# Kernel optimization log

Hardware: AMD Instinct MI355X
Metric: run time of the kernel (lower is better)

Reference implementation:

```python
import jax, jax.numpy as jnp
import numpy as np

N, D = 4096, 2048

def setup_inputs() -> dict:
    key = jax.random.key(0)
    k1, k2 = jax.random.split(key)
    Ws = jax.random.normal(k1, (N, D), dtype=jnp.float32)
    # nn.Bilinear(D, D, 1): weight [1, D, D], bias [1]
    W = jax.random.normal(k2, (1, D, D), dtype=jnp.float32) * (1.0 / np.sqrt(D))
    b = jnp.zeros((1,), dtype=jnp.float32)
    return {"Ws": Ws, "W": W, "b": b}

def reference(Ws, W, b):
    # A[i, j] = Ws[i] @ W[0] @ Ws[j] + b[0]  (bilinear score for every pair)
    t = Ws @ W[0]                 # [N, D]
    A = t @ Ws.T + b[0]           # [N, N]
    return jax.nn.softmax(A, axis=1)
```

## Files before the change

### kernel.cpp

```cpp
#include <hip/hip_runtime.h>

typedef __bf16 bf16x8 __attribute__((ext_vector_type(8)));
typedef float f32x4 __attribute__((ext_vector_type(4)));
typedef unsigned short u16;
typedef u16 u16x8 __attribute__((ext_vector_type(8)));

#define AS1 __attribute__((address_space(1)))
#define AS3 __attribute__((address_space(3)))
#define MF(d, a, b) d = __builtin_amdgcn_mfma_f32_16x16x32_bf16(a, b, d, 0, 0, 0)

__device__ __forceinline__ void split2(float x, u16& h, u16& l) {
  __bf16 hb = (__bf16)x;
  float hf = (float)hb;
  __bf16 lb = (__bf16)(x - hf);
  h = __builtin_bit_cast(u16, hb);
  l = __builtin_bit_cast(u16, lb);
}

__global__ __launch_bounds__(256) void k_pack_ws(const float* __restrict__ X,
                                                 u16* __restrict__ P) {
  const int total8 = (4096 * 2048) / 8;
  for (int idx = blockIdx.x * 256 + threadIdx.x; idx < total8; idx += gridDim.x * 256) {
    int row = idx >> 8;
    int k8  = idx & 255;
    const float* src = X + ((size_t)row << 11) + (k8 << 3);
    const float4 v0 = *(const float4*)src;
    const float4 v1 = *(const float4*)(src + 4);
    float xv[8] = {v0.x, v0.y, v0.z, v0.w, v1.x, v1.y, v1.z, v1.w};
    u16x8 hv, lv;
#pragma unroll
    for (int j = 0; j < 8; ++j) { u16 h, l; split2(xv[j], h, l); hv[j] = h; lv[j] = l; }
    size_t base = ((size_t)row << 12) + (size_t)((k8 >> 2) << 6) + ((k8 & 3) << 3);
    *(u16x8*)(P + base) = hv;
    *(u16x8*)(P + base + 32) = lv;
  }
}

__global__ __launch_bounds__(256) void k_transpose_pack_w(const float* __restrict__ W,
                                                          u16* __restrict__ P) {
  __shared__ float tile[32][33];
  const int tx = threadIdx.x, ty = threadIdx.y;
  const int kbase = blockIdx.y << 5, cbase = blockIdx.x << 5;
#pragma unroll
  for (int i = 0; i < 4; ++i)
    tile[ty * 4 + i][tx] = W[((size_t)(kbase + ty * 4 + i) << 11) + cbase + tx];
  __syncthreads();
#pragma unroll
  for (int i = 0; i < 4; ++i) {
    int c = cbase + ty * 4 + i;
    float v = tile[tx][ty * 4 + i];
    u16 h, l; split2(v, h, l);
    size_t base = ((size_t)c << 12) + (size_t)(kbase << 1) + tx;
    P[base] = h;
    P[base + 32] = l;
  }
}

__global__ __launch_bounds__(256, 2) void k_gemm_nt(const u16* __restrict__ Ap,
                                                    const u16* __restrict__ Bp,
                                                    u16* __restrict__ Cpack) {
  __shared__ __align__(16) u16 lds_a[128 * 64];
  __shared__ __align__(16) u16 lds_b[128 * 64];
  const int bid = blockIdx.x;
  const int swzb = (bid & 7) * 64 + (bid >> 3);
  const int bx = swzb & 15, by = swzb >> 4;
  const int tid = threadIdx.x;
  const int lane = tid & 63, w = tid >> 6;
  const int wr = w >> 1, wc = w & 1;
  const int row0 = by << 7, col0 = bx << 7;
  const int lrow = lane & 15, kg = lane >> 4;

  f32x4 acc[4][4] = {};

  const u16* abase = Ap + ((size_t)row0 << 12);
  const u16* bbase = Bp + ((size_t)col0 << 12);

  int offAh[4], offAl[4], offBh[4], offBl[4];
#pragma unroll
  for (int m = 0; m < 4; ++m) {
    int r = wr * 64 + m * 16 + lrow;
    int sw = r & 7;
    offAh[m] = r * 64 + ((kg ^ sw) << 3);
    offAl[m] = r * 64 + (((4 + kg) ^ sw) << 3);
    int rb = wc * 64 + m * 16 + lrow;
    int swb = rb & 7;
    offBh[m] = rb * 64 + ((kg ^ swb) << 3);
    offBl[m] = rb * 64 + (((4 + kg) ^ swb) << 3);
  }

  for (int kb = 0; kb < 64; ++kb) {
    const int kofs = kb << 6;
#pragma unroll
    for (int i = 0; i < 4; ++i) {
      int s = i * 256 + tid;
      int r = s >> 3, c = s & 7;
      int cs = c ^ (r & 7);
      __builtin_amdgcn_global_load_lds(
          (const AS1 unsigned int*)(abase + ((size_t)r << 12) + kofs + (cs << 3)),
          (AS3 unsigned int*)(lds_a + ((i * 256 + w * 64) << 3)), 16, 0, 0);
    }
#pragma unroll
    for (int i = 0; i < 4; ++i) {
      int s = i * 256 + tid;
      int r = s >> 3, c = s & 7;
      int cs = c ^ (r & 7);
      __builtin_amdgcn_global_load_lds(
          (const AS1 unsigned int*)(bbase + ((size_t)r << 12) + kofs + (cs << 3)),
          (AS3 unsigned int*)(lds_b + ((i * 256 + w * 64) << 3)), 16, 0, 0);
    }
    __syncthreads();

    bf16x8 ah[4], al[4];
#pragma unroll
    for (int m = 0; m < 4; ++m) {
      ah[m] = *(const bf16x8*)&lds_a[offAh[m]];
      al[m] = *(const bf16x8*)&lds_a[offAl[m]];
    }
#pragma unroll
    for (int n = 0; n < 4; ++n) {
      bf16x8 bh = *(const bf16x8*)&lds_b[offBh[n]];
      bf16x8 bl = *(const bf16x8*)&lds_b[offBl[n]];
#pragma unroll
      for (int m = 0; m < 4; ++m) {
        MF(acc[m][n], ah[m], bh);
        MF(acc[m][n], ah[m], bl);
        MF(acc[m][n], al[m], bh);
      }
    }
    __syncthreads();
  }

#pragma unroll
  for (int m = 0; m < 4; ++m) {
#pragma unroll
    for (int n = 0; n < 4; ++n) {
#pragma unroll
      for (int j = 0; j < 4; ++j) {
        int gr = row0 + wr * 64 + m * 16 + kg * 4 + j;
        int gc = col0 + wc * 64 + n * 16 + lrow;
        u16 h, l; split2(acc[m][n][j], h, l);
        size_t base = ((size_t)gr << 12) + (size_t)((gc >> 5) << 6) + (gc & 31);
        Cpack[base] = h;
        Cpack[base + 32] = l;
      }
    }
  }
}

__global__ __launch_bounds__(512, 2) void k_gemm256(const u16* __restrict__ Ap,
                                                    const u16* __restrict__ Bp,
                                                    float* __restrict__ Cout) {
  __shared__ __align__(16) u16 smA[32768];
  const int bid = blockIdx.x;
  const int swzb = (bid & 7) * 32 + (bid >> 3);
  const int bx = swzb & 15, by = swzb >> 4;
  const int tid = threadIdx.x;
  const int lane = tid & 63, w = tid >> 6;
  const int wr = w >> 2, wc = w & 3;
  const int row0 = by << 8, col0 = bx << 8;
  const int lrow = lane & 15, kg = lane >> 4;
  const int sw = lrow & 7;

  const u16* Abase = Ap + ((size_t)row0 << 12);
  const u16* Bbase = Bp + ((size_t)col0 << 12);

  const size_t gsrc0 = ((size_t)(tid >> 3) << 12) + ((size_t)((tid & 7) ^ ((tid >> 3) & 7)) << 3);
  const int dst0 = (w * 64) << 3;

  auto stA = [&](int T, int j) {
    __builtin_amdgcn_global_load_lds(
        (const AS1 unsigned int*)(Abase + gsrc0 + ((size_t)(j * 64) << 12) + ((T & 63) << 6)),
        (AS3 unsigned int*)(smA + ((T & 1) << 14) + j * 4096 + dst0), 16, 0, 0);
  };
  auto ldB = [&](int T, bf16x8* BH, bf16x8* BL) {
    const u16* src = Bbase + ((T & 63) << 6) + (kg << 3);
#pragma unroll
    for (int n = 0; n < 4; ++n) {
      size_t c = (size_t)(wc * 64 + n * 16 + lrow) << 12;
      BH[n] = *(const bf16x8*)(src + c);
      BL[n] = *(const bf16x8*)(src + c + 32);
    }
  };

  const int baseAh = (wr * 128 + lrow) * 64 + ((kg ^ sw) << 3);
  const int baseAl = (wr * 128 + lrow) * 64 + (((4 | kg) ^ sw) << 3);

  f32x4 acc[8][4] = {};
  bf16x8 bhE[4], blE[4], bhO[4], blO[4];

  stA(0, 0); stA(0, 1); stA(0, 2); stA(0, 3);
  ldB(0, bhE, blE);
  ldB(1, bhO, blO);
  __builtin_amdgcn_sched_barrier(0);
  asm volatile("s_waitcnt vmcnt(8)" ::: "memory");
  __builtin_amdgcn_sched_barrier(0);
  __builtin_amdgcn_s_barrier();

  for (int i = 0; i < 32; ++i) {
    const int t0 = 2 * i;
    const u16* laE = smA;
    const u16* laO = smA + 16384;
#pragma unroll
    for (int q = 0; q < 4; ++q) {
      bf16x8 a0h = *(const bf16x8*)&laE[baseAh + (2 * q) * 1024];
      bf16x8 a0l = *(const bf16x8*)&laE[baseAl + (2 * q) * 1024];
      bf16x8 a1h = *(const bf16x8*)&laE[baseAh + (2 * q + 1) * 1024];
      bf16x8 a1l = *(const bf16x8*)&laE[baseAl + (2 * q + 1) * 1024];
      if (q == 0) { stA(t0 + 1, 0); stA(t0 + 1, 1); }
      if (q == 1) { stA(t0 + 1, 2); stA(t0 + 1, 3); }
      __builtin_amdgcn_s_barrier();
      __builtin_amdgcn_s_setprio(1);
      const int m0 = 2 * q, m1 = 2 * q + 1;
#pragma unroll
      for (int n = 0; n < 4; ++n) { MF(acc[m0][n], a0h, bhE[n]); MF(acc[m1][n], a1h, bhE[n]); }
#pragma unroll
      for (int n = 0; n < 4; ++n) { MF(acc[m0][n], a0h, blE[n]); MF(acc[m1][n], a1h, blE[n]); }
#pragma unroll
      for (int n = 0; n < 4; ++n) { MF(acc[m0][n], a0l, bhE[n]); MF(acc[m1][n], a1l, bhE[n]); }
      __builtin_amdgcn_s_setprio(0);
      if (q == 3) {
        ldB(t0 + 2, bhE, blE);
        __builtin_amdgcn_sched_barrier(0);
        asm volatile("s_waitcnt vmcnt(8)" ::: "memory");
        __builtin_amdgcn_sched_barrier(0);
      }
      __builtin_amdgcn_s_barrier();
    }
#pragma unroll
    for (int q = 0; q < 4; ++q) {
      bf16x8 a0h = *(const bf16x8*)&laO[baseAh + (2 * q) * 1024];
      bf16x8 a0l = *(const bf16x8*)&laO[baseAl + (2 * q) * 1024];
      bf16x8 a1h = *(const bf16x8*)&laO[baseAh + (2 * q + 1) * 1024];
      bf16x8 a1l = *(const bf16x8*)&laO[baseAl + (2 * q + 1) * 1024];
      if (q == 0) { stA(t0 + 2, 0); stA(t0 + 2, 1); }
      if (q == 1) { stA(t0 + 2, 2); stA(t0 + 2, 3); }
      __builtin_amdgcn_s_barrier();
      __builtin_amdgcn_s_setprio(1);
      const int m0 = 2 * q, m1 = 2 * q + 1;
#pragma unroll
      for (int n = 0; n < 4; ++n) { MF(acc[m0][n], a0h, bhO[n]); MF(acc[m1][n], a1h, bhO[n]); }
#pragma unroll
      for (int n = 0; n < 4; ++n) { MF(acc[m0][n], a0h, blO[n]); MF(acc[m1][n], a1h, blO[n]); }
#pragma unroll
      for (int n = 0; n < 4; ++n) { MF(acc[m0][n], a0l, bhO[n]); MF(acc[m1][n], a1l, bhO[n]); }
      __builtin_amdgcn_s_setprio(0);
      if (q == 3) {
        ldB(t0 + 3, bhO, blO);
        __builtin_amdgcn_sched_barrier(0);
        asm volatile("s_waitcnt vmcnt(8)" ::: "memory");
        __builtin_amdgcn_sched_barrier(0);
      }
      __builtin_amdgcn_s_barrier();
    }
  }
  asm volatile("s_waitcnt vmcnt(0)" ::: "memory");

#pragma unroll
  for (int m = 0; m < 8; ++m) {
#pragma unroll
    for (int n = 0; n < 4; ++n) {
#pragma unroll
      for (int j = 0; j < 4; ++j) {
        int gr = row0 + wr * 128 + m * 16 + kg * 4 + j;
        int gc = col0 + wc * 64 + n * 16 + lrow;
        Cout[((size_t)gr << 12) + gc] = acc[m][n][j];
      }
    }
  }
}

__global__ __launch_bounds__(256) void k_softmax_rows(float* __restrict__ A) {
  const int row = blockIdx.x;
  float* p = A + ((size_t)row << 12);
  const int tid = threadIdx.x;
  const int lane = tid & 63, w = tid >> 6;
  float4 v[4];
  float mx = -3.0e38f;
#pragma unroll
  for (int i = 0; i < 4; ++i) {
    v[i] = ((const float4*)p)[tid + (i << 8)];
    mx = fmaxf(mx, fmaxf(fmaxf(v[i].x, v[i].y), fmaxf(v[i].z, v[i].w)));
  }
#pragma unroll
  for (int off = 32; off; off >>= 1) mx = fmaxf(mx, __shfl_xor(mx, off, 64));
  __shared__ float redm[4], reds[4];
  if (lane == 0) redm[w] = mx;
  __syncthreads();
  mx = fmaxf(fmaxf(redm[0], redm[1]), fmaxf(redm[2], redm[3]));
  float s = 0.f;
#pragma unroll
  for (int i = 0; i < 4; ++i) {
    v[i].x = __expf(v[i].x - mx);
    v[i].y = __expf(v[i].y - mx);
    v[i].z = __expf(v[i].z - mx);
    v[i].w = __expf(v[i].w - mx);
    s += (v[i].x + v[i].y) + (v[i].z + v[i].w);
  }
#pragma unroll
  for (int off = 32; off; off >>= 1) s += __shfl_xor(s, off, 64);
  if (lane == 0) reds[w] = s;
  __syncthreads();
  s = (reds[0] + reds[1]) + (reds[2] + reds[3]);
  const float inv = 1.0f / s;
#pragma unroll
  for (int i = 0; i < 4; ++i) {
    v[i].x *= inv; v[i].y *= inv; v[i].z *= inv; v[i].w *= inv;
    ((float4*)p)[tid + (i << 8)] = v[i];
  }
}

extern "C" void kernel_launch(void* const* d_in, const int* in_sizes, int n_in,
                              void* d_out, int out_size, void* d_ws, size_t ws_size,
                              hipStream_t stream) {
  (void)in_sizes; (void)n_in; (void)out_size; (void)ws_size;
  const float* Ws = (const float*)d_in[0];
  const float* W  = (const float*)d_in[1];
  float* out = (float*)d_out;

  u16* ws_pack = (u16*)d_ws;
  u16* wt_pack = ws_pack + (size_t)4096 * 4096;
  u16* t_pack  = wt_pack + (size_t)2048 * 4096;

  k_pack_ws<<<4096, 256, 0, stream>>>(Ws, ws_pack);
  k_transpose_pack_w<<<dim3(64, 64), dim3(32, 8), 0, stream>>>(W, wt_pack);
  k_gemm_nt<<<512, 256, 0, stream>>>(ws_pack, wt_pack, t_pack);
  k_gemm256<<<256, 512, 0, stream>>>(t_pack, ws_pack, out);
  k_softmax_rows<<<4096, 256, 0, stream>>>(out);
}
```

Measured before the change: 322.5 us.

## Replace 256x256 gemm with 128x256 tile staging both operands through LDS

```diff
diff --git a/kernel.cpp b/kernel.cpp
--- a/kernel.cpp
+++ b/kernel.cpp
@@ -147,17 +147,18 @@
   }
 }
 
-__global__ __launch_bounds__(512, 2) void k_gemm256(const u16* __restrict__ Ap,
-                                                    const u16* __restrict__ Bp,
-                                                    float* __restrict__ Cout) {
-  __shared__ __align__(16) u16 smA[32768];
+__global__ __launch_bounds__(512, 4) void k_gemm2(const u16* __restrict__ Ap,
+                                                  const u16* __restrict__ Bp,
+                                                  float* __restrict__ Cout) {
+  __shared__ __align__(16) u16 smA[16384];
+  __shared__ __align__(16) u16 smB[16384];
   const int bid = blockIdx.x;
-  const int swzb = (bid & 7) * 32 + (bid >> 3);
+  const int swzb = (bid & 7) * 64 + (bid >> 3);
   const int bx = swzb & 15, by = swzb >> 4;
   const int tid = threadIdx.x;
   const int lane = tid & 63, w = tid >> 6;
   const int wr = w >> 2, wc = w & 3;
-  const int row0 = by << 8, col0 = bx << 8;
+  const int row0 = by << 7, col0 = bx << 8;
   const int lrow = lane & 15, kg = lane >> 4;
   const int sw = lrow & 7;
 
@@ -165,103 +166,79 @@
   const u16* Bbase = Bp + ((size_t)col0 << 12);
 
   const size_t gsrc0 = ((size_t)(tid >> 3) << 12) + ((size_t)((tid & 7) ^ ((tid >> 3) & 7)) << 3);
-  const int dst0 = (w * 64) << 3;
+  const int dst0 = w * 512;
 
   auto stA = [&](int T, int j) {
     __builtin_amdgcn_global_load_lds(
         (const AS1 unsigned int*)(Abase + gsrc0 + ((size_t)(j * 64) << 12) + ((T & 63) << 6)),
-        (AS3 unsigned int*)(smA + ((T & 1) << 14) + j * 4096 + dst0), 16, 0, 0);
+        (AS3 unsigned int*)(smA + ((T & 1) << 13) + j * 4096 + dst0), 16, 0, 0);
   };
-  auto ldB = [&](int T, bf16x8* BH, bf16x8* BL) {
-    const u16* src = Bbase + ((T & 63) << 6) + (kg << 3);
-#pragma unroll
-    for (int n = 0; n < 4; ++n) {
-      size_t c = (size_t)(wc * 64 + n * 16 + lrow) << 12;
-      BH[n] = *(const bf16x8*)(src + c);
-      BL[n] = *(const bf16x8*)(src + c + 32);
-    }
+  auto stB = [&](int T, int u) {
+    __builtin_amdgcn_global_load_lds(
+        (const AS1 unsigned int*)(Bbase + gsrc0 + ((size_t)(u * 64) << 12) + ((T & 63) << 6)),
+        (AS3 unsigned int*)(smB + u * 4096 + dst0), 16, 0, 0);
   };
 
-  const int baseAh = (wr * 128 + lrow) * 64 + ((kg ^ sw) << 3);
-  const int baseAl = (wr * 128 + lrow) * 64 + (((4 | kg) ^ sw) << 3);
-
-  f32x4 acc[8][4] = {};
-  bf16x8 bhE[4], blE[4], bhO[4], blO[4];
-
-  stA(0, 0); stA(0, 1); stA(0, 2); stA(0, 3);
-  ldB(0, bhE, blE);
-  ldB(1, bhO, blO);
-  __builtin_amdgcn_sched_barrier(0);
-  asm volatile("s_waitcnt vmcnt(8)" ::: "memory");
+  const int baseAh = (wr * 64 + lrow) * 64 + ((kg ^ sw) << 3);
+  const int baseAl = (wr * 64 + lrow) * 64 + (((4 | kg) ^ sw) << 3);
+  int offBh[4], offBl[4];
+#pragma unroll
+  for (int n = 0; n < 4; ++n) {
+    offBh[n] = (wc * 64 + n * 16 + lrow) * 64 + ((kg ^ sw) << 3);
+    offBl[n] = (wc * 64 + n * 16 + lrow) * 64 + (((4 | kg) ^ sw) << 3);
+  }
+
+  f32x4 acc[4][4] = {};
+  bf16x8 bh[4], bl[4];
+
+  stA(0, 0); stA(0, 1);
+  stB(0, 0); stB(0, 1); stB(0, 2); stB(0, 3);
+  asm volatile("s_waitcnt vmcnt(0)" ::: "memory");
   __builtin_amdgcn_sched_barrier(0);
   __builtin_amdgcn_s_barrier();
 
-  for (int i = 0; i < 32; ++i) {
-    const int t0 = 2 * i;
-    const u16* laE = smA;
-    const u16* laO = smA + 16384;
+  for (int t = 0; t < 64; ++t) {
+    const u16* abuf = smA + ((t & 1) << 13);
 #pragma unroll
     for (int q = 0; q < 4; ++q) {
-      bf16x8 a0h = *(const bf16x8*)&laE[baseAh + (2 * q) * 1024];
-      bf16x8 a0l = *(const bf16x8*)&laE[baseAl + (2 * q) * 1024];
-      bf16x8 a1h = *(const bf16x8*)&laE[baseAh + (2 * q + 1) * 1024];
-      bf16x8 a1l = *(const bf16x8*)&laE[baseAl + (2 * q + 1) * 1024];
-      if (q == 0) { stA(t0 + 1, 0); stA(t0 + 1, 1); }
-      if (q == 1) { stA(t0 + 1, 2); stA(t0 + 1, 3); }
+      if (q == 0) {
+#pragma unroll
+        for (int n = 0; n < 4; ++n) {
+          bh[n] = *(const bf16x8*)&smB[offBh[n]];
+          bl[n] = *(const bf16x8*)&smB[offBl[n]];
+        }
+      }
+      bf16x8 ah = *(const bf16x8*)&abuf[baseAh + q * 1024];
+      bf16x8 al = *(const bf16x8*)&abuf[baseAl + q * 1024];
+      if (q == 0) { stA(t + 1, 0); stA(t + 1, 1); }
+      if (q == 1) { stB(t + 1, 0); stB(t + 1, 1); }
+      if (q == 2) { stB(t + 1, 2); stB(t + 1, 3); }
       __builtin_amdgcn_s_barrier();
       __builtin_amdgcn_s_setprio(1);
-      const int m0 = 2 * q, m1 = 2 * q + 1;
-#pragma unroll
-      for (int n = 0; n < 4; ++n) { MF(acc[m0][n], a0h, bhE[n]); MF(acc[m1][n], a1h, bhE[n]); }
-#pragma unroll
-      for (int n = 0; n < 4; ++n) { MF(acc[m0][n], a0h, blE[n]); MF(acc[m1][n], a1h, blE[n]); }
-#pragma unroll
-      for (int n = 0; n < 4; ++n) { MF(acc[m0][n], a0l, bhE[n]); MF(acc[m1][n], a1l, bhE[n]); }
+#pragma unroll
+      for (int n = 0; n < 4; ++n) MF(acc[q][n], ah, bh[n]);
+#pragma unroll
+      for (int n = 0; n < 4; ++n) MF(acc[q][n], ah, bl[n]);
+#pragma unroll
+      for (int n = 0; n < 4; ++n) MF(acc[q][n], al, bh[n]);
       __builtin_amdgcn_s_setprio(0);
+      asm volatile("s_waitcnt lgkmcnt(0)" ::: "memory");
+      __builtin_amdgcn_sched_barrier(0);
       if (q == 3) {
-        ldB(t0 + 2, bhE, blE);
+        asm volatile("s_waitcnt vmcnt(0)" ::: "memory");
         __builtin_amdgcn_sched_barrier(0);
-        asm volatile("s_waitcnt vmcnt(8)" ::: "memory");
-        __builtin_amdgcn_sched_barrier(0);
       }
       __builtin_amdgcn_s_barrier();
     }
-#pragma unroll
-    for (int q = 0; q < 4; ++q) {
-      bf16x8 a0h = *(const bf16x8*)&laO[baseAh + (2 * q) * 1024];
-      bf16x8 a0l = *(const bf16x8*)&laO[baseAl + (2 * q) * 1024];
-      bf16x8 a1h = *(const bf16x8*)&laO[baseAh + (2 * q + 1) * 1024];
-      bf16x8 a1l = *(const bf16x8*)&laO[baseAl + (2 * q + 1) * 1024];
-      if (q == 0) { stA(t0 + 2, 0); stA(t0 + 2, 1); }
-      if (q == 1) { stA(t0 + 2, 2); stA(t0 + 2, 3); }
-      __builtin_amdgcn_s_barrier();
-      __builtin_amdgcn_s_setprio(1);
-      const int m0 = 2 * q, m1 = 2 * q + 1;
-#pragma unroll
-      for (int n = 0; n < 4; ++n) { MF(acc[m0][n], a0h, bhO[n]); MF(acc[m1][n], a1h, bhO[n]); }
-#pragma unroll
-      for (int n = 0; n < 4; ++n) { MF(acc[m0][n], a0h, blO[n]); MF(acc[m1][n], a1h, blO[n]); }
-#pragma unroll
-      for (int n = 0; n < 4; ++n) { MF(acc[m0][n], a0l, bhO[n]); MF(acc[m1][n], a1l, bhO[n]); }
-      __builtin_amdgcn_s_setprio(0);
-      if (q == 3) {
-        ldB(t0 + 3, bhO, blO);
-        __builtin_amdgcn_sched_barrier(0);
-        asm volatile("s_waitcnt vmcnt(8)" ::: "memory");
-        __builtin_amdgcn_sched_barrier(0);
-      }
-      __builtin_amdgcn_s_barrier();
-    }
-  }
-  asm volatile("s_waitcnt vmcnt(0)" ::: "memory");
-
-#pragma unroll
-  for (int m = 0; m < 8; ++m) {
+  }
+
+#pragma unroll
+  for (int m = 0; m < 4; ++m) {
 #pragma unroll
     for (int n = 0; n < 4; ++n) {
 #pragma unroll
       for (int j = 0; j < 4; ++j) {
-        int gr = row0 + wr * 128 + m * 16 + kg * 4 + j;
+        int gr = row0 + wr * 64 + m * 16 + kg * 4 + j;
         int gc = col0 + wc * 64 + n * 16 + lrow;
         Cout[((size_t)gr << 12) + gc] = acc[m][n][j];
       }
@@ -324,6 +301,6 @@
   k_pack_ws<<<4096, 256, 0, stream>>>(Ws, ws_pack);
   k_transpose_pack_w<<<dim3(64, 64), dim3(32, 8), 0, stream>>>(W, wt_pack);
   k_gemm_nt<<<512, 256, 0, stream>>>(ws_pack, wt_pack, t_pack);
-  k_gemm256<<<256, 512, 0, stream>>>(t_pack, ws_pack, out);
+  k_gemm2<<<512, 512, 0, stream>>>(t_pack, ws_pack, out);
   k_softmax_rows<<<4096, 256, 0, stream>>>(out);
 }
```

Result: faster. 298.1 us (-7.6%).
